# Kernel optimization log

Hardware: AMD Instinct MI355X
Metric: run time of the kernel (lower is better)

Reference implementation:

```python
import jax, jax.numpy as jnp
import numpy as np

B, T = 4, 2048
N_EMBED = 1536
N_HEADS = 24
KV_HEADS = 8
HEAD_DIM = 64
REPEAT = N_HEADS // KV_HEADS  # 3, hardcoded in the torch module's .repeat(1,1,3)
D = REPEAT * HEAD_DIM         # per-group attention dim = 192 (RoPE dim)
THETA = 10000.0


def rope_tables(t_len):
    # angles: (D/2,), positions: (t_len,) -> (t_len, D/2)
    angles = 1.0 / (THETA ** (jnp.arange(0, D, 2, dtype=jnp.float32) / D))
    th = jnp.arange(t_len, dtype=jnp.float32)[:, None] * angles[None, :]
    return jnp.cos(th), jnp.sin(th)


def apply_rope(x, cos, sin):
    # x: (..., T, D); consecutive pairs (even, odd) form complex numbers,
    # rotated by e^{i * t * theta_j} (torch.view_as_complex semantics).
    xr = x[..., 0::2]
    xi = x[..., 1::2]
    yr = xr * cos - xi * sin
    yi = xr * sin + xi * cos
    return jnp.stack([yr, yi], axis=-1).reshape(x.shape)


def setup_inputs() -> dict:
    key = jax.random.key(0)
    ks = jax.random.split(key, 7)
    s = 0.02
    return {
        "x":  jax.random.normal(ks[0], (B, T, N_EMBED), dtype=jnp.float32),
        "Wq": jax.random.normal(ks[1], (N_EMBED, N_HEADS * HEAD_DIM), dtype=jnp.float32) * s,
        "bq": jnp.zeros((N_HEADS * HEAD_DIM,), dtype=jnp.float32),
        "Wk": jax.random.normal(ks[2], (N_EMBED, KV_HEADS * HEAD_DIM), dtype=jnp.float32) * s,
        "bk": jnp.zeros((KV_HEADS * HEAD_DIM,), dtype=jnp.float32),
        "Wv": jax.random.normal(ks[3], (N_EMBED, KV_HEADS * HEAD_DIM), dtype=jnp.float32) * s,
        "bv": jnp.zeros((KV_HEADS * HEAD_DIM,), dtype=jnp.float32),
    }


def reference(x, Wq, bq, Wk, bk, Wv, bv):
    # projections
    q = x @ Wq + bq   # (B,T,KV_HEADS*D)
    k = x @ Wk + bk   # (B,T,KV_HEADS*HEAD_DIM)
    v = x @ Wv + bv

    # split into kv-groups; each group is ONE attention head of dim D
    q = q.reshape(B, T, KV_HEADS, D).transpose(0, 2, 1, 3)          # (B,G,T,D)
    k = k.reshape(B, T, KV_HEADS, HEAD_DIM).transpose(0, 2, 1, 3)   # (B,G,T,hd)
    v = v.reshape(B, T, KV_HEADS, HEAD_DIM).transpose(0, 2, 1, 3)

    # torch .repeat(1,1,3): concat 3 copies along channel dim
    k = jnp.tile(k, (1, 1, 1, REPEAT))  # (B,G,T,D)
    v = jnp.tile(v, (1, 1, 1, REPEAT))

    cos, sin = rope_tables(T)  # (T, D/2)
    q = apply_rope(q, cos, sin)
    k = apply_rope(k, cos, sin)

    scale = 1.0 / jnp.sqrt(jnp.asarray(D, dtype=q.dtype))
    scores = jnp.einsum("bgqd,bgkd->bgqk", q, k) * scale  # (B,G,T,T)
    causal = jnp.tril(jnp.ones((T, T), dtype=bool))
    scores = jnp.where(causal, scores, -jnp.inf)
    p = jax.nn.softmax(scores, axis=-1)
    out = jnp.einsum("bgqk,bgkd->bgqd", p, v)             # (B,G,T,D)
    return out.transpose(0, 2, 1, 3).reshape(B, T, N_EMBED)
```

## Files before the change

kernel.cpp:

```cpp
#include <hip/hip_runtime.h>
#include <hip/hip_bf16.h>

#define TT 2048
#define EMB 1536
#define NQK 2560
#define DD 192
#define NPAIR 96

typedef __attribute__((ext_vector_type(8))) __bf16 bf16x8;
typedef __attribute__((ext_vector_type(4))) float f32x4;

#define MFMA16(a,b,c) __builtin_amdgcn_mfma_f32_16x16x32_bf16((a),(b),(c),0,0,0)

__device__ __forceinline__ void lds_load16(const void* g, void* l) {
  __builtin_amdgcn_global_load_lds(
      (const __attribute__((address_space(1))) void*)g,
      (__attribute__((address_space(3))) void*)l, 16, 0, 0);
}

__global__ __launch_bounds__(256) void k_tables(float* __restrict__ cosT,
                                                float* __restrict__ sinT) {
  int i = blockIdx.x * 256 + threadIdx.x;
  int t = i / NPAIR, p = i % NPAIR;
  float invf = powf(10000.0f, -(2.0f * p) / 192.0f);
  float th = (float)t * invf;
  cosT[i] = cosf(th);
  sinT[i] = sinf(th);
}

__global__ __launch_bounds__(256) void k_cvt(const float4* __restrict__ in,
                                             ushort4* __restrict__ outp) {
  int i = blockIdx.x * 256 + threadIdx.x;
  float4 v = in[i];
  __hip_bfloat16 h0 = __float2bfloat16(v.x), h1 = __float2bfloat16(v.y);
  __hip_bfloat16 h2 = __float2bfloat16(v.z), h3 = __float2bfloat16(v.w);
  ushort4 o;
  o.x = *(unsigned short*)&h0; o.y = *(unsigned short*)&h1;
  o.z = *(unsigned short*)&h2; o.w = *(unsigned short*)&h3;
  outp[i] = o;
}

__global__ __launch_bounds__(256) void k_tw(const float* __restrict__ Wq,
                                            const float* __restrict__ Wk,
                                            const float* __restrict__ Wv,
                                            __hip_bfloat16* __restrict__ Wt) {
  __shared__ float tile[32][33];
  int n0 = blockIdx.x * 32;
  int k0 = blockIdx.y * 32;
  int tx = threadIdx.x & 31, ty = threadIdx.x >> 5;
#pragma unroll
  for (int i = 0; i < 4; ++i) {
    int k = k0 + ty + 8 * i;
    int n = n0 + tx;
    float v;
    if (n < 1536)      v = Wq[(size_t)k * 1536 + n];
    else if (n < 2048) v = Wk[(size_t)k * 512 + (n - 1536)];
    else               v = Wv[(size_t)k * 512 + (n - 2048)];
    tile[ty + 8 * i][tx] = v;
  }
  __syncthreads();
#pragma unroll
  for (int i = 0; i < 4; ++i) {
    int n = n0 + ty + 8 * i;
    int k = k0 + tx;
    Wt[(size_t)n * 1536 + k] = __float2bfloat16(tile[tx][ty + 8 * i]);
  }
}

__global__ __launch_bounds__(256, 2) void k_gemm(const __hip_bfloat16* __restrict__ A,
                                                 const __hip_bfloat16* __restrict__ Bt,
                                                 const float* __restrict__ bq,
                                                 const float* __restrict__ bk,
                                                 const float* __restrict__ bv,
                                                 __hip_bfloat16* __restrict__ C) {
  extern __shared__ __align__(16) char smraw[];
  const int tid = threadIdx.x;
  const int lane = tid & 63;
  const int l15 = lane & 15, lh = lane >> 4;
  const int wid = tid >> 6;
  const int bid = blockIdx.x;
  const int n0 = (bid & 7) * 320;
  const int m0 = (bid >> 3) * 128;

  const __hip_bfloat16* Ab = A + (size_t)m0 * 1536;
  const __hip_bfloat16* Bb = Bt + (size_t)n0 * 1536;

  int goff[7], ldst[7];
#pragma unroll
  for (int j = 0; j < 7; ++j) {
    int i = ((j < 2) ? j : (j - 2)) * 256 + tid;
    int line = i >> 3, half = (i >> 2) & 1, s16 = i & 3;
    int row = (line << 1) | half;
    int s = s16 ^ (line & 3);
    goff[j] = row * 1536 + s * 8;
    ldst[j] = ((j < 2) ? 0 : 8192) + i * 16;
  }

  f32x4 acc[8][5];
#pragma unroll
  for (int i = 0; i < 8; ++i)
#pragma unroll
    for (int j = 0; j < 5; ++j) acc[i][j] = (f32x4){0.f, 0.f, 0.f, 0.f};

  auto stage = [&](int t) {
    char* base = smraw + (t & 1) * 28672;
    const int k0 = t * 32;
    lds_load16(Ab + goff[0] + k0, base + ldst[0]);
    lds_load16(Ab + goff[1] + k0, base + ldst[1]);
#pragma unroll
    for (int j = 2; j < 7; ++j)
      lds_load16(Bb + goff[j] + k0, base + ldst[j]);
  };
  auto ardA = [&](const char* sb, int fi) -> bf16x8 {
    int r = fi * 16 + l15;
    int byte = ((r >> 1) << 7) + ((r & 1) << 6) + ((lh ^ ((r >> 1) & 3)) << 4);
    return *(const bf16x8*)(sb + byte);
  };
  auto ardB = [&](const char* sb, int fj) -> bf16x8 {
    int r = wid * 80 + fj * 16 + l15;
    int byte = ((r >> 1) << 7) + ((r & 1) << 6) + ((lh ^ ((r >> 1) & 3)) << 4);
    return *(const bf16x8*)(sb + 8192 + byte);
  };

  stage(0);

  for (int t = 0; t < 48; ++t) {
    const char* sb = smraw + (t & 1) * 28672;
    if (t < 47) {
      stage(t + 1);
      asm volatile("s_waitcnt vmcnt(7)" ::: "memory");
    } else {
      asm volatile("s_waitcnt vmcnt(0)" ::: "memory");
    }
    __builtin_amdgcn_sched_barrier(0);
    __builtin_amdgcn_s_barrier();

    bf16x8 bfr[5], a0[4], a1[4];
#pragma unroll
    for (int fj = 0; fj < 5; ++fj) bfr[fj] = ardB(sb, fj);
#pragma unroll
    for (int fi = 0; fi < 4; ++fi) a0[fi] = ardA(sb, fi);
    __builtin_amdgcn_sched_barrier(0);
#pragma unroll
    for (int fi = 0; fi < 4; ++fi) a1[fi] = ardA(sb, fi + 4);
    __builtin_amdgcn_sched_barrier(0);

    asm volatile("s_waitcnt lgkmcnt(4)" ::: "memory");
    __builtin_amdgcn_sched_barrier(0);
    __builtin_amdgcn_s_setprio(1);
#pragma unroll
    for (int fi = 0; fi < 4; ++fi)
#pragma unroll
      for (int fj = 0; fj < 5; ++fj)
        acc[fi][fj] = MFMA16(a0[fi], bfr[fj], acc[fi][fj]);
    __builtin_amdgcn_s_setprio(0);

    asm volatile("s_waitcnt lgkmcnt(0)" ::: "memory");
    __builtin_amdgcn_sched_barrier(0);
    __builtin_amdgcn_s_setprio(1);
#pragma unroll
    for (int fi = 0; fi < 4; ++fi)
#pragma unroll
      for (int fj = 0; fj < 5; ++fj)
        acc[fi + 4][fj] = MFMA16(a1[fi], bfr[fj], acc[fi + 4][fj]);
    __builtin_amdgcn_s_setprio(0);
    __builtin_amdgcn_s_barrier();
  }

#pragma unroll
  for (int fj = 0; fj < 5; ++fj) {
    int n = n0 + wid * 80 + fj * 16 + l15;
    float bias = (n < 1536) ? bq[n] : (n < 2048) ? bk[n - 1536] : bv[n - 2048];
#pragma unroll
    for (int fi = 0; fi < 8; ++fi)
#pragma unroll
      for (int r = 0; r < 4; ++r) {
        int mrow = m0 + fi * 16 + lh * 4 + r;
        C[(size_t)mrow * NQK + n] = __float2bfloat16(acc[fi][fj][r] + bias);
      }
  }
}

__global__ __launch_bounds__(256) void k_rope(const __hip_bfloat16* __restrict__ QKV,
                                              const float* __restrict__ cosT,
                                              const float* __restrict__ sinT,
                                              __hip_bfloat16* __restrict__ qrp,
                                              __hip_bfloat16* __restrict__ krp) {
  int row = blockIdx.x;
  int b = row >> 11, t = row & 2047;
  __shared__ float cs[NPAIR], sn[NPAIR];
  int tid = threadIdx.x;
  if (tid < NPAIR) { cs[tid] = cosT[t * NPAIR + tid]; sn[tid] = sinT[t * NPAIR + tid]; }
  __syncthreads();
  const __hip_bfloat16* src = QKV + (size_t)row * NQK;
  const float sc = 0.07216878364870323f;
  for (int i = tid; i < 768; i += 256) {
    int g = i / NPAIR, p = i % NPAIR;
    float xr = __bfloat162float(src[g * DD + 2 * p]);
    float xi = __bfloat162float(src[g * DD + 2 * p + 1]);
    float c = cs[p], s = sn[p];
    size_t o = ((size_t)(b * 8 + g) * TT + t) * DD + 2 * p;
    qrp[o]     = __float2bfloat16((xr * c - xi * s) * sc);
    qrp[o + 1] = __float2bfloat16((xr * s + xi * c) * sc);
  }
  for (int i = tid; i < 768; i += 256) {
    int g = i / NPAIR, p = i % NPAIR;
    int j = (2 * p) & 63;
    float xr = __bfloat162float(src[1536 + g * 64 + j]);
    float xi = __bfloat162float(src[1536 + g * 64 + j + 1]);
    float c = cs[p], s = sn[p];
    size_t o = ((size_t)(b * 8 + g) * TT + t) * DD + 2 * p;
    krp[o]     = __float2bfloat16(xr * c - xi * s);
    krp[o + 1] = __float2bfloat16(xr * s + xi * c);
  }
}

__global__ __launch_bounds__(256) void k_tv(const __hip_bfloat16* __restrict__ QKV,
                                            __hip_bfloat16* __restrict__ vt) {
  __shared__ __align__(16) __hip_bfloat16 tile[64][72];
  int bg = blockIdx.y;
  int b = bg >> 3, g = bg & 7;
  int t0 = blockIdx.x * 64;
  int tid = threadIdx.x;
  {
    int r = tid >> 2, c0 = (tid & 3) * 16;
    const __hip_bfloat16* src =
        QKV + (size_t)(b * TT + t0 + r) * NQK + 2048 + g * 64 + c0;
    *(bf16x8*)&tile[r][c0] = *(const bf16x8*)src;
    *(bf16x8*)&tile[r][c0 + 8] = *(const bf16x8*)(src + 8);
  }
  __syncthreads();
  {
    int vd = tid >> 2, c0 = (tid & 3) * 16;
    __hip_bfloat16 o0[8], o1[8];
#pragma unroll
    for (int i = 0; i < 8; ++i) { o0[i] = tile[c0 + i][vd]; o1[i] = tile[c0 + 8 + i][vd]; }
    __hip_bfloat16* dst = vt + ((size_t)bg * 64 + vd) * TT + t0 + c0;
    *(bf16x8*)dst = *(bf16x8*)o0;
    *(bf16x8*)(dst + 8) = *(bf16x8*)o1;
  }
}

__global__ __launch_bounds__(256) void k_attn(const __hip_bfloat16* __restrict__ qrp,
                                              const __hip_bfloat16* __restrict__ krp,
                                              const __hip_bfloat16* __restrict__ vt,
                                              float* __restrict__ out) {
  __shared__ __align__(16) char Ksh[2][24576];
  __shared__ __align__(16) char Vsh[2][8192];
  __shared__ __align__(16) __hip_bfloat16 Plds[4][16 * 72];

  const int tid = threadIdx.x, lane = tid & 63, wid = tid >> 6;
  const int l15 = lane & 15, lh = lane >> 4;
  const int bg = blockIdx.x;
  const int qt = (int)(gridDim.y - 1) - (int)blockIdx.y;
  const int b = bg >> 3, g = bg & 7;
  const int q0 = qt * 64;
  const int qw = q0 + wid * 16;

  const __hip_bfloat16* Qb = qrp + ((size_t)bg * TT + qw) * DD;
  bf16x8 aq[6];
#pragma unroll
  for (int kc = 0; kc < 6; ++kc)
    aq[kc] = *(const bf16x8*)(Qb + l15 * DD + kc * 32 + lh * 8);

  bf16x8 vones;
#pragma unroll
  for (int j = 0; j < 8; ++j) vones[j] = (__bf16)1.0f;

  f32x4 oacc[4];
#pragma unroll
  for (int c = 0; c < 4; ++c) oacc[c] = (f32x4){0.f, 0.f, 0.f, 0.f};
  f32x4 sacc = (f32x4){0.f, 0.f, 0.f, 0.f};

  __hip_bfloat16* P = &Plds[wid][0];
  const __hip_bfloat16* Kbase = krp + (size_t)bg * TT * DD;
  const __hip_bfloat16* Vbase = vt + (size_t)bg * 64 * TT;

  auto stage = [&](int bsel, int kv0) {
    char* Kd = Ksh[bsel];
#pragma unroll
    for (int j = 0; j < 6; ++j) {
      int i = wid * 384 + j * 64 + lane;
      int row = i / 24;
      int s = i - row * 24;
      int gsl = (s & 0x18) | ((s ^ row) & 7);
      lds_load16(Kbase + (size_t)(kv0 + row) * DD + gsl * 8, Kd + i * 16);
    }
    char* Vd = Vsh[bsel];
#pragma unroll
    for (int j = 0; j < 2; ++j) {
      int i = wid * 128 + j * 64 + lane;
      int row = i >> 3;
      int s = i & 7;
      int gsl = s ^ (row & 7);
      lds_load16(Vbase + (size_t)row * TT + kv0 + gsl * 8, Vd + i * 16);
    }
  };

  const int nt = qt + 1;
  int buf = 0;
  stage(0, 0);

  for (int it = 0; it < nt; ++it) {
    const int kv0 = it * 64;
    if (it + 1 < nt) {
      stage(buf ^ 1, kv0 + 64);
      asm volatile("s_waitcnt vmcnt(8)" ::: "memory");
    } else {
      asm volatile("s_waitcnt vmcnt(0)" ::: "memory");
    }
    __builtin_amdgcn_sched_barrier(0);
    __builtin_amdgcn_s_barrier();

    const char* Kl = Ksh[buf];
    f32x4 s[4];
#pragma unroll
    for (int c = 0; c < 4; ++c) s[c] = (f32x4){0.f, 0.f, 0.f, 0.f};
#pragma unroll
    for (int kc = 0; kc < 6; ++kc) {
#pragma unroll
      for (int c = 0; c < 4; ++c) {
        int row = c * 16 + l15;
        int sl = kc * 4 + lh;
        int sw = (sl & 0x18) | ((sl ^ row) & 7);
        bf16x8 bk = *(const bf16x8*)(Kl + row * 384 + sw * 16);
        s[c] = MFMA16(aq[kc], bk, s[c]);
      }
    }
    if (kv0 == q0) {
      const int qrel = wid * 16 + lh * 4;
#pragma unroll
      for (int c = 0; c < 4; ++c) {
        const int kpos = c * 16 + l15;
#pragma unroll
        for (int r = 0; r < 4; ++r) {
          float p = (kpos > qrel + r) ? 0.f : __expf(s[c][r]);
          P[(lh * 4 + r) * 72 + c * 16 + l15] = __float2bfloat16(p);
        }
      }
    } else {
#pragma unroll
      for (int c = 0; c < 4; ++c)
#pragma unroll
        for (int r = 0; r < 4; ++r)
          P[(lh * 4 + r) * 72 + c * 16 + l15] = __float2bfloat16(__expf(s[c][r]));
    }
    asm volatile("" ::: "memory");
    __builtin_amdgcn_sched_barrier(0);
    const char* Vl = Vsh[buf];
#pragma unroll
    for (int k2 = 0; k2 < 2; ++k2) {
      bf16x8 pa = *(const bf16x8*)(P + l15 * 72 + k2 * 32 + lh * 8);
      sacc = MFMA16(pa, vones, sacc);
#pragma unroll
      for (int c = 0; c < 4; ++c) {
        int row = c * 16 + l15;
        int sl = k2 * 4 + lh;
        int sw = (sl ^ row) & 7;
        bf16x8 bv = *(const bf16x8*)(Vl + row * 128 + sw * 16);
        oacc[c] = MFMA16(pa, bv, oacc[c]);
      }
    }
    asm volatile("" ::: "memory");
    __builtin_amdgcn_sched_barrier(0);
    __builtin_amdgcn_s_barrier();
    buf ^= 1;
  }
  float inv[4];
#pragma unroll
  for (int r = 0; r < 4; ++r) inv[r] = 1.0f / sacc[r];
#pragma unroll
  for (int r = 0; r < 4; ++r) {
    const int t = qw + lh * 4 + r;
    float* orow = out + ((size_t)b * TT + t) * EMB + g * DD;
#pragma unroll
    for (int c = 0; c < 4; ++c) {
      float v = oacc[c][r] * inv[r];
      orow[c * 16 + l15] = v;
      orow[64 + c * 16 + l15] = v;
      orow[128 + c * 16 + l15] = v;
    }
  }
}

extern "C" void kernel_launch(void* const* d_in, const int* in_sizes, int n_in,
                              void* d_out, int out_size, void* d_ws, size_t ws_size,
                              hipStream_t stream) {
  const float* x  = (const float*)d_in[0];
  const float* Wq = (const float*)d_in[1];
  const float* bq = (const float*)d_in[2];
  const float* Wk = (const float*)d_in[3];
  const float* bk = (const float*)d_in[4];
  const float* Wv = (const float*)d_in[5];
  const float* bv = (const float*)d_in[6];
  float* out = (float*)d_out;
  char* ws = (char*)d_ws;

  float*          cosT = (float*)(ws);
  float*          sinT = (float*)(ws + 786432);
  __hip_bfloat16* xb   = (__hip_bfloat16*)(ws + 1572864);
  __hip_bfloat16* qrp  = (__hip_bfloat16*)(ws + 1572864);
  __hip_bfloat16* wtb  = (__hip_bfloat16*)(ws + 26738688);
  __hip_bfloat16* qkv  = (__hip_bfloat16*)(ws + 34603008);
  __hip_bfloat16* krp  = (__hip_bfloat16*)(ws + 76546048);
  __hip_bfloat16* vt   = (__hip_bfloat16*)(ws + 101711872);

  k_tables<<<768, 256, 0, stream>>>(cosT, sinT);
  k_cvt<<<12288, 256, 0, stream>>>((const float4*)x, (ushort4*)xb);
  k_tw<<<dim3(80, 48), 256, 0, stream>>>(Wq, Wk, Wv, wtb);
  k_gemm<<<512, 256, 57344, stream>>>(xb, wtb, bq, bk, bv, qkv);
  k_tv<<<dim3(32, 32), 256, 0, stream>>>(qkv, vt);
  k_rope<<<8192, 256, 0, stream>>>(qkv, cosT, sinT, qrp, krp);
  k_attn<<<dim3(32, 32), 256, 0, stream>>>(qrp, krp, vt, out);
}
```

Before: 179.0 us.

## Double query tile per attention block and single-buffer V with split waits

The attention kernel now processes 128 query rows per block, with each wave handling two 16-row subtiles, so every staged K/V tile is reused across twice as many queries and the grid halves. V is now single-buffered and its next tile is loaded only after the barrier at the end of each iteration, with separate vmcnt waits for K and V. This cuts LDS use and global traffic per query, but it adds registers, halves the block count, which may hurt occupancy and load balance, and leaves the V load less overlapped. The RoPE table kernel also swaps powf for exp2f, a negligible change.

```diff
diff --git a/kernel.cpp b/kernel.cpp
--- a/kernel.cpp
+++ b/kernel.cpp
@@ -22,7 +22,7 @@
                                                 float* __restrict__ sinT) {
   int i = blockIdx.x * 256 + threadIdx.x;
   int t = i / NPAIR, p = i % NPAIR;
-  float invf = powf(10000.0f, -(2.0f * p) / 192.0f);
+  float invf = exp2f((float)p * (-13.287712379549449f / 96.0f));
   float th = (float)t * invf;
   cosT[i] = cosf(th);
   sinT[i] = sinf(th);
@@ -246,37 +246,43 @@
                                               const __hip_bfloat16* __restrict__ vt,
                                               float* __restrict__ out) {
   __shared__ __align__(16) char Ksh[2][24576];
-  __shared__ __align__(16) char Vsh[2][8192];
-  __shared__ __align__(16) __hip_bfloat16 Plds[4][16 * 72];
+  __shared__ __align__(16) char Vsh[8192];
+  __shared__ __align__(16) __hip_bfloat16 Plds[4][32 * 72];
 
   const int tid = threadIdx.x, lane = tid & 63, wid = tid >> 6;
   const int l15 = lane & 15, lh = lane >> 4;
   const int bg = blockIdx.x;
   const int qt = (int)(gridDim.y - 1) - (int)blockIdx.y;
   const int b = bg >> 3, g = bg & 7;
-  const int q0 = qt * 64;
-  const int qw = q0 + wid * 16;
+  const int q0 = qt * 128;
+  const int qw = q0 + wid * 32;
 
   const __hip_bfloat16* Qb = qrp + ((size_t)bg * TT + qw) * DD;
-  bf16x8 aq[6];
-#pragma unroll
-  for (int kc = 0; kc < 6; ++kc)
-    aq[kc] = *(const bf16x8*)(Qb + l15 * DD + kc * 32 + lh * 8);
+  bf16x8 aq[2][6];
+#pragma unroll
+  for (int s = 0; s < 2; ++s)
+#pragma unroll
+    for (int kc = 0; kc < 6; ++kc)
+      aq[s][kc] = *(const bf16x8*)(Qb + (s * 16 + l15) * DD + kc * 32 + lh * 8);
 
   bf16x8 vones;
 #pragma unroll
   for (int j = 0; j < 8; ++j) vones[j] = (__bf16)1.0f;
 
-  f32x4 oacc[4];
-#pragma unroll
-  for (int c = 0; c < 4; ++c) oacc[c] = (f32x4){0.f, 0.f, 0.f, 0.f};
-  f32x4 sacc = (f32x4){0.f, 0.f, 0.f, 0.f};
+  f32x4 oacc[2][4];
+#pragma unroll
+  for (int s = 0; s < 2; ++s)
+#pragma unroll
+    for (int c = 0; c < 4; ++c) oacc[s][c] = (f32x4){0.f, 0.f, 0.f, 0.f};
+  f32x4 sacc[2];
+  sacc[0] = (f32x4){0.f, 0.f, 0.f, 0.f};
+  sacc[1] = (f32x4){0.f, 0.f, 0.f, 0.f};
 
   __hip_bfloat16* P = &Plds[wid][0];
   const __hip_bfloat16* Kbase = krp + (size_t)bg * TT * DD;
   const __hip_bfloat16* Vbase = vt + (size_t)bg * 64 * TT;
 
-  auto stage = [&](int bsel, int kv0) {
+  auto stageK = [&](int bsel, int kv0) {
     char* Kd = Ksh[bsel];
 #pragma unroll
     for (int j = 0; j < 6; ++j) {
@@ -286,36 +292,39 @@
       int gsl = (s & 0x18) | ((s ^ row) & 7);
       lds_load16(Kbase + (size_t)(kv0 + row) * DD + gsl * 8, Kd + i * 16);
     }
-    char* Vd = Vsh[bsel];
+  };
+  auto stageV = [&](int kv0) {
 #pragma unroll
     for (int j = 0; j < 2; ++j) {
       int i = wid * 128 + j * 64 + lane;
       int row = i >> 3;
       int s = i & 7;
       int gsl = s ^ (row & 7);
-      lds_load16(Vbase + (size_t)row * TT + kv0 + gsl * 8, Vd + i * 16);
+      lds_load16(Vbase + (size_t)row * TT + kv0 + gsl * 8, Vsh + i * 16);
     }
   };
 
-  const int nt = qt + 1;
-  int buf = 0;
-  stage(0, 0);
+  const int nt = 2 * qt + 2;
+  stageK(0, 0);
+  stageV(0);
 
   for (int it = 0; it < nt; ++it) {
     const int kv0 = it * 64;
     if (it + 1 < nt) {
-      stage(buf ^ 1, kv0 + 64);
+      stageK((it + 1) & 1, kv0 + 64);
       asm volatile("s_waitcnt vmcnt(8)" ::: "memory");
     } else {
-      asm volatile("s_waitcnt vmcnt(0)" ::: "memory");
+      asm volatile("s_waitcnt vmcnt(2)" ::: "memory");
     }
     __builtin_amdgcn_sched_barrier(0);
     __builtin_amdgcn_s_barrier();
 
-    const char* Kl = Ksh[buf];
-    f32x4 s[4];
-#pragma unroll
-    for (int c = 0; c < 4; ++c) s[c] = (f32x4){0.f, 0.f, 0.f, 0.f};
+    const char* Kl = Ksh[it & 1];
+    f32x4 sc_[2][4];
+#pragma unroll
+    for (int s = 0; s < 2; ++s)
+#pragma unroll
+      for (int c = 0; c < 4; ++c) sc_[s][c] = (f32x4){0.f, 0.f, 0.f, 0.f};
 #pragma unroll
     for (int kc = 0; kc < 6; ++kc) {
 #pragma unroll
@@ -324,63 +333,79 @@
         int sl = kc * 4 + lh;
         int sw = (sl & 0x18) | ((sl ^ row) & 7);
         bf16x8 bk = *(const bf16x8*)(Kl + row * 384 + sw * 16);
-        s[c] = MFMA16(aq[kc], bk, s[c]);
+        sc_[0][c] = MFMA16(aq[0][kc], bk, sc_[0][c]);
+        sc_[1][c] = MFMA16(aq[1][kc], bk, sc_[1][c]);
       }
     }
-    if (kv0 == q0) {
-      const int qrel = wid * 16 + lh * 4;
-#pragma unroll
-      for (int c = 0; c < 4; ++c) {
-        const int kpos = c * 16 + l15;
-#pragma unroll
-        for (int r = 0; r < 4; ++r) {
-          float p = (kpos > qrel + r) ? 0.f : __expf(s[c][r]);
-          P[(lh * 4 + r) * 72 + c * 16 + l15] = __float2bfloat16(p);
+    if (it >= nt - 2) {
+#pragma unroll
+      for (int s = 0; s < 2; ++s)
+#pragma unroll
+        for (int c = 0; c < 4; ++c) {
+          const int kpos = kv0 + c * 16 + l15;
+#pragma unroll
+          for (int r = 0; r < 4; ++r) {
+            const int qabs = qw + s * 16 + lh * 4 + r;
+            float p = (kpos > qabs) ? 0.f : __expf(sc_[s][c][r]);
+            P[(s * 16 + lh * 4 + r) * 72 + c * 16 + l15] = __float2bfloat16(p);
+          }
+        }
+    } else {
+#pragma unroll
+      for (int s = 0; s < 2; ++s)
+#pragma unroll
+        for (int c = 0; c < 4; ++c)
+#pragma unroll
+          for (int r = 0; r < 4; ++r)
+            P[(s * 16 + lh * 4 + r) * 72 + c * 16 + l15] =
+                __float2bfloat16(__expf(sc_[s][c][r]));
+    }
+    if (it + 1 < nt) {
+      asm volatile("s_waitcnt vmcnt(6)" ::: "memory");
+    } else {
+      asm volatile("s_waitcnt vmcnt(0)" ::: "memory");
+    }
+    __builtin_amdgcn_sched_barrier(0);
+#pragma unroll
+    for (int s = 0; s < 2; ++s) {
+#pragma unroll
+      for (int k2 = 0; k2 < 2; ++k2) {
+        bf16x8 pa = *(const bf16x8*)(P + (s * 16 + l15) * 72 + k2 * 32 + lh * 8);
+        sacc[s] = MFMA16(pa, vones, sacc[s]);
+#pragma unroll
+        for (int c = 0; c < 4; ++c) {
+          int row = c * 16 + l15;
+          int sl = k2 * 4 + lh;
+          int sw = (sl ^ row) & 7;
+          bf16x8 bv = *(const bf16x8*)(Vsh + row * 128 + sw * 16);
+          oacc[s][c] = MFMA16(pa, bv, oacc[s][c]);
         }
       }
-    } else {
-#pragma unroll
-      for (int c = 0; c < 4; ++c)
-#pragma unroll
-        for (int r = 0; r < 4; ++r)
-          P[(lh * 4 + r) * 72 + c * 16 + l15] = __float2bfloat16(__expf(s[c][r]));
     }
     asm volatile("" ::: "memory");
     __builtin_amdgcn_sched_barrier(0);
-    const char* Vl = Vsh[buf];
-#pragma unroll
-    for (int k2 = 0; k2 < 2; ++k2) {
-      bf16x8 pa = *(const bf16x8*)(P + l15 * 72 + k2 * 32 + lh * 8);
-      sacc = MFMA16(pa, vones, sacc);
+    __builtin_amdgcn_s_barrier();
+    if (it + 1 < nt) stageV(kv0 + 64);
+  }
+  float inv[2][4];
+#pragma unroll
+  for (int s = 0; s < 2; ++s)
+#pragma unroll
+    for (int r = 0; r < 4; ++r) inv[s][r] = 1.0f / sacc[s][r];
+#pragma unroll
+  for (int s = 0; s < 2; ++s)
+#pragma unroll
+    for (int r = 0; r < 4; ++r) {
+      const int t = qw + s * 16 + lh * 4 + r;
+      float* orow = out + ((size_t)b * TT + t) * EMB + g * DD;
 #pragma unroll
       for (int c = 0; c < 4; ++c) {
-        int row = c * 16 + l15;
-        int sl = k2 * 4 + lh;
-        int sw = (sl ^ row) & 7;
-        bf16x8 bv = *(const bf16x8*)(Vl + row * 128 + sw * 16);
-        oacc[c] = MFMA16(pa, bv, oacc[c]);
+        float v = oacc[s][c][r] * inv[s][r];
+        orow[c * 16 + l15] = v;
+        orow[64 + c * 16 + l15] = v;
+        orow[128 + c * 16 + l15] = v;
       }
     }
-    asm volatile("" ::: "memory");
-    __builtin_amdgcn_sched_barrier(0);
-    __builtin_amdgcn_s_barrier();
-    buf ^= 1;
-  }
-  float inv[4];
-#pragma unroll
-  for (int r = 0; r < 4; ++r) inv[r] = 1.0f / sacc[r];
-#pragma unroll
-  for (int r = 0; r < 4; ++r) {
-    const int t = qw + lh * 4 + r;
-    float* orow = out + ((size_t)b * TT + t) * EMB + g * DD;
-#pragma unroll
-    for (int c = 0; c < 4; ++c) {
-      float v = oacc[c][r] * inv[r];
-      orow[c * 16 + l15] = v;
-      orow[64 + c * 16 + l15] = v;
-      orow[128 + c * 16 + l15] = v;
-    }
-  }
 }
 
 extern "C" void kernel_launch(void* const* d_in, const int* in_sizes, int n_in,
@@ -411,5 +436,5 @@
   k_gemm<<<512, 256, 57344, stream>>>(xb, wtb, bq, bk, bv, qkv);
   k_tv<<<dim3(32, 32), 256, 0, stream>>>(qkv, vt);
   k_rope<<<8192, 256, 0, stream>>>(qkv, cosT, sinT, qrp, krp);
-  k_attn<<<dim3(32, 32), 256, 0, stream>>>(qrp, krp, vt, out);
-}
+  k_attn<<<dim3(32, 16), 256, 0, stream>>>(qrp, krp, vt, out);
+}
```

Measured after the change: 186.2 us. +4.0%, slower.
